# Kernel optimization log

Hardware: AMD Instinct MI355X
Metric: run time of the kernel (lower is better)

The kernel has to match this reference:

```python
import jax, jax.numpy as jnp
import numpy as np

D_CONV = 4
D_STATE = 16
DT_RANK = 64


def _silu(x):
    return x * jax.nn.sigmoid(x)


def setup_inputs() -> dict:
    key = jax.random.key(0)
    ks = jax.random.split(key, 10)
    B, L, dim = 2, 1024, 1024
    d_inner = 2 * dim
    s = lambda fan: 1.0 / np.sqrt(fan)
    inp = {
        "x": jax.random.normal(ks[0], (B, L, dim), jnp.float32),
        "ln_w": jnp.ones((dim,), jnp.float32),
        "ln_b": jnp.zeros((dim,), jnp.float32),
        "w_in": jax.random.normal(ks[1], (2 * d_inner, dim), jnp.float32) * s(dim),
        "conv_w": jax.random.normal(ks[2], (d_inner, D_CONV), jnp.float32) * s(D_CONV),
        "conv_b": jnp.zeros((d_inner,), jnp.float32),
        "w_xproj": jax.random.normal(ks[3], (DT_RANK + 2 * D_STATE, d_inner), jnp.float32) * s(d_inner),
        "w_dt": jax.random.normal(ks[4], (d_inner, DT_RANK), jnp.float32) * s(DT_RANK),
        "b_dt": jax.random.normal(ks[5], (d_inner,), jnp.float32) * 0.1,
        # S4D-real init: A = -(1..d_state) per channel
        "a_log": jnp.tile(jnp.log(jnp.arange(1, D_STATE + 1, dtype=jnp.float32)), (d_inner, 1)),
        "d_skip": jnp.ones((d_inner,), jnp.float32),
        "w_out": jax.random.normal(ks[6], (dim, d_inner), jnp.float32) * s(d_inner),
    }
    return inp


def reference(x, ln_w, ln_b, w_in, conv_w, conv_b, w_xproj, w_dt, b_dt, a_log, d_skip, w_out):
    B, L, dim = x.shape
    residual = x

    # LayerNorm
    mu = jnp.mean(x, axis=-1, keepdims=True)
    var = jnp.mean((x - mu) ** 2, axis=-1, keepdims=True)
    xn = (x - mu) * jax.lax.rsqrt(var + 1e-5) * ln_w + ln_b

    # in_proj -> (x_ssm, z) each (B, L, d_inner)
    xz = jnp.einsum("bld,ed->ble", xn, w_in)
    d_inner = xz.shape[-1] // 2
    xs, z = xz[..., :d_inner], xz[..., d_inner:]

    # depthwise causal conv1d (kernel D_CONV) + SiLU
    xp = jnp.pad(xs, ((0, 0), (D_CONV - 1, 0), (0, 0)))
    xc = conv_b
    for k in range(D_CONV):
        xc = xc + conv_w[:, k] * xp[:, k : k + L, :]
    u = _silu(xc)  # (B, L, d_inner)

    # x_proj -> dt, B, C
    x_dbl = jnp.einsum("ble,re->blr", u, w_xproj)
    dt_r = x_dbl[..., :DT_RANK]
    B_ssm = x_dbl[..., DT_RANK : DT_RANK + D_STATE]         # (B, L, n)
    C_ssm = x_dbl[..., DT_RANK + D_STATE :]                 # (B, L, n)

    dt = jax.nn.softplus(jnp.einsum("blr,er->ble", dt_r, w_dt) + b_dt)  # (B, L, d_inner)

    A = -jnp.exp(a_log)  # (d_inner, n)
    deltaA = jnp.exp(jnp.einsum("ble,en->blen", dt, A))            # (B, L, e, n)
    deltaBu = jnp.einsum("ble,bln,ble->blen", dt, B_ssm, u)        # (B, L, e, n)

    # selective scan over L
    def step(h, ins):
        dA_t, dBu_t, C_t = ins
        h = dA_t * h + dBu_t                       # (B, e, n)
        y = jnp.einsum("ben,bn->be", h, C_t)
        return h, y

    h0 = jnp.zeros((B, d_inner, D_STATE), xs.dtype)
    _, ys = jax.lax.scan(
        step,
        h0,
        (deltaA.transpose(1, 0, 2, 3), deltaBu.transpose(1, 0, 2, 3), C_ssm.transpose(1, 0, 2)),
    )
    y = ys.transpose(1, 0, 2) + u * d_skip         # (B, L, e)

    y = y * _silu(z)
    out = jnp.einsum("ble,de->bld", y, w_out)
    return residual + out
```

## Files before the change

kernel.cpp:

```cpp
#include <hip/hip_runtime.h>
#include <hip/hip_bf16.h>


#define LC 32
#define NCHUNK 32

typedef short bf16x8 __attribute__((ext_vector_type(8)));
typedef float f32x4  __attribute__((ext_vector_type(4)));

static __device__ __forceinline__ float siluf(float x) { return x / (1.f + __expf(-x)); }
static __device__ __forceinline__ unsigned short f2bf(float f) {
    unsigned int u = __float_as_uint(f);
    unsigned int r = (u + 0x7fffu + ((u >> 16) & 1u)) >> 16;
    return (unsigned short)r;
}
static __device__ __forceinline__ float bfb(unsigned short u) {
    return __uint_as_float(((unsigned int)u) << 16);
}
static __device__ __forceinline__ void gload_lds16(const void* g, void* l) {
    __builtin_amdgcn_global_load_lds(
        (const __attribute__((address_space(1))) void*)g,
        (__attribute__((address_space(3))) void*)l, 16, 0, 0);
}

__global__ __launch_bounds__(256) void f2b_all(
    const float* __restrict__ w_in,  unsigned short* __restrict__ w_in_b,
    const float* __restrict__ w_out, unsigned short* __restrict__ w_out_b,
    const float* __restrict__ w_dt,  unsigned short* __restrict__ w_dt_b)
{
    int i = blockIdx.x * 256 + threadIdx.x;
    const float* in; unsigned short* outp; int j;
    if (i < 1048576)      { in = w_in;  outp = w_in_b;  j = i; }
    else if (i < 1572864) { in = w_out; outp = w_out_b; j = i - 1048576; }
    else if (i < 1605632) { in = w_dt;  outp = w_dt_b;  j = i - 1572864; }
    else return;
    float4 v = reinterpret_cast<const float4*>(in)[j];
    ushort4 o = { f2bf(v.x), f2bf(v.y), f2bf(v.z), f2bf(v.w) };
    reinterpret_cast<ushort4*>(outp)[j] = o;
}

__global__ __launch_bounds__(256) void ln_kernel(
    const float* __restrict__ x,
    const float* __restrict__ w,
    const float* __restrict__ bias,
    unsigned short* __restrict__ xn)
{
    int m = blockIdx.x, tid = threadIdx.x;
    const float4* xr = reinterpret_cast<const float4*>(x) + (size_t)m * 256;
    float4 r = xr[tid];
    float f0 = r.x, f1 = r.y, f2 = r.z, f3 = r.w;
    float s  = f0 + f1 + f2 + f3;
    float s2 = f0*f0 + f1*f1 + f2*f2 + f3*f3;
    #pragma unroll
    for (int off = 32; off > 0; off >>= 1) {
        s  += __shfl_down(s, off);
        s2 += __shfl_down(s2, off);
    }
    __shared__ float red[8];
    if ((tid & 63) == 0) { red[tid >> 6] = s; red[4 + (tid >> 6)] = s2; }
    __syncthreads();
    float st = red[0] + red[1] + red[2] + red[3];
    float qt = red[4] + red[5] + red[6] + red[7];
    float mu   = st * (1.f / 1024.f);
    float var  = qt * (1.f / 1024.f) - mu * mu;
    float rstd = rsqrtf(var + 1e-5f);
    float4 wv = reinterpret_cast<const float4*>(w)[tid];
    float4 bv = reinterpret_cast<const float4*>(bias)[tid];
    ushort4 o = { f2bf((f0 - mu) * rstd * wv.x + bv.x),
                  f2bf((f1 - mu) * rstd * wv.y + bv.y),
                  f2bf((f2 - mu) * rstd * wv.z + bv.z),
                  f2bf((f3 - mu) * rstd * wv.w + bv.w) };
    reinterpret_cast<ushort4*>(xn + (size_t)m * 1024)[tid] = o;
}

__global__ __launch_bounds__(256) void gemm_bf16_nt(
    const unsigned short* __restrict__ A, int lda,
    const unsigned short* __restrict__ B, int ldb,
    int Kslice,
    float* __restrict__ C, unsigned short* __restrict__ Cb, int ldc,
    const float* __restrict__ bias,
    int ep, size_t Cstride)
{
    __shared__ short As[2 * 128 * 32];
    __shared__ short Bs[2 * 64 * 32];
    int tid = threadIdx.x;
    int z = blockIdx.z;
    A += (size_t)z * Kslice;
    B += (size_t)z * Kslice;
    C += (size_t)z * Cstride;
    int m0 = blockIdx.y * 128, n0 = blockIdx.x * 64;
    int lane = tid & 63, wave = tid >> 6;
    int wm = (wave >> 1) * 64, wn = (wave & 1) * 32;
    int frow = lane & 15, fq = lane >> 4;

    f32x4 acc[4][2] = {};

    int lrow = lane >> 2;
    int scol = (lane & 3) * 8;
    const unsigned short* AgL = A + (size_t)(m0 + wave * 32 + lrow) * lda + scol;
    const unsigned short* BgL = B + (size_t)(n0 + wave * 16 + lrow) * ldb + scol;
    int aoff = (wave * 32) * 32;
    int boff = (wave * 16) * 32;

    gload_lds16(AgL,                      As + aoff);
    gload_lds16(AgL + (size_t)16 * lda,   As + aoff + 16 * 32);
    gload_lds16(BgL,                      Bs + boff);

    int cur = 0;
    for (int k0 = 0; k0 < Kslice; k0 += 32) {
        __syncthreads();
        int nk = k0 + 32;
        if (nk < Kslice) {
            int nxt = cur ^ 1;
            gload_lds16(AgL + nk,                     As + nxt * 4096 + aoff);
            gload_lds16(AgL + (size_t)16 * lda + nk,  As + nxt * 4096 + aoff + 16 * 32);
            gload_lds16(BgL + nk,                     Bs + nxt * 2048 + boff);
        }
        const short* Ac = As + cur * 4096;
        const short* Bc = Bs + cur * 2048;
        bf16x8 af[4], bfr[2];
        #pragma unroll
        for (int i = 0; i < 4; ++i)
            af[i] = *reinterpret_cast<const bf16x8*>(Ac + (wm + i * 16 + frow) * 32 + fq * 8);
        #pragma unroll
        for (int j = 0; j < 2; ++j)
            bfr[j] = *reinterpret_cast<const bf16x8*>(Bc + (wn + j * 16 + frow) * 32 + fq * 8);
        #pragma unroll
        for (int i = 0; i < 4; ++i)
            #pragma unroll
            for (int j = 0; j < 2; ++j)
                acc[i][j] = __builtin_amdgcn_mfma_f32_16x16x32_bf16(af[i], bfr[j], acc[i][j], 0, 0, 0);
        cur ^= 1;
    }

    int cn = lane & 15, rq = (lane >> 4) * 4;
    #pragma unroll
    for (int i = 0; i < 4; ++i) {
        #pragma unroll
        for (int j = 0; j < 2; ++j) {
            #pragma unroll
            for (int r = 0; r < 4; ++r) {
                int row = m0 + wm + i * 16 + rq + r;
                int col = n0 + wn + j * 16 + cn;
                float v = acc[i][j][r];
                if (ep == 0) {
                    C[(size_t)row * ldc + col] = v;
                } else if (ep == 1) {
                    v += bias[col];
                    v = (v > 20.f) ? v : log1pf(__expf(v));
                    Cb[(size_t)row * ldc + col] = f2bf(v);
                } else {
                    Cb[(size_t)row * ldc + col] = f2bf(v);
                }
            }
        }
    }
}

__global__ __launch_bounds__(256) void out_reduce(
    const float* __restrict__ part, const float* __restrict__ x,
    float* __restrict__ out)
{
    int i = blockIdx.x * 256 + threadIdx.x;
    float4 s = reinterpret_cast<const float4*>(x)[i];
    #pragma unroll
    for (int z = 0; z < 4; ++z) {
        float4 p = reinterpret_cast<const float4*>(part + (size_t)z * 2097152)[i];
        s.x += p.x; s.y += p.y; s.z += p.z; s.w += p.w;
    }
    reinterpret_cast<float4*>(out)[i] = s;
}

__global__ __launch_bounds__(256) void xproj_splitk(
    const unsigned short* __restrict__ A,
    const float* __restrict__ B,
    float* __restrict__ part)
{
    __shared__ float As[16][68];
    __shared__ float Bs[16][100];
    int tid = threadIdx.x;
    int m0 = blockIdx.x * 64;
    int k0 = blockIdx.y * 128;
    int tx = tid & 15;
    int ty = tid >> 4;
    float acc[4][6] = {};
    int arow = tid >> 2, akg = (tid & 3) << 2;
    int brow1 = (256 + tid) >> 2, bkg1 = ((256 + tid) & 3) << 2;

    for (int ks = 0; ks < 128; ks += 16) {
        ushort4 au = *reinterpret_cast<const ushort4*>(A + (size_t)(m0 + arow) * 2048 + k0 + ks + akg);
        float4 av = make_float4(bfb(au.x), bfb(au.y), bfb(au.z), bfb(au.w));
        float4 bv0 = make_float4(0.f, 0.f, 0.f, 0.f), bv1 = bv0;
        if (arow < 96)  bv0 = *reinterpret_cast<const float4*>(B + (size_t)arow * 2048 + k0 + ks + akg);
        if (brow1 < 96) bv1 = *reinterpret_cast<const float4*>(B + (size_t)brow1 * 2048 + k0 + ks + bkg1);
        __syncthreads();
        As[akg + 0][arow] = av.x; As[akg + 1][arow] = av.y;
        As[akg + 2][arow] = av.z; As[akg + 3][arow] = av.w;
        if (arow < 96) {
            Bs[akg + 0][arow] = bv0.x; Bs[akg + 1][arow] = bv0.y;
            Bs[akg + 2][arow] = bv0.z; Bs[akg + 3][arow] = bv0.w;
        }
        if (brow1 < 96) {
            Bs[bkg1 + 0][brow1] = bv1.x; Bs[bkg1 + 1][brow1] = bv1.y;
            Bs[bkg1 + 2][brow1] = bv1.z; Bs[bkg1 + 3][brow1] = bv1.w;
        }
        __syncthreads();
        #pragma unroll
        for (int k = 0; k < 16; ++k) {
            float aa[4], bb[6];
            #pragma unroll
            for (int i = 0; i < 4; ++i) aa[i] = As[k][ty * 4 + i];
            #pragma unroll
            for (int j = 0; j < 6; ++j) bb[j] = Bs[k][tx * 6 + j];
            #pragma unroll
            for (int i = 0; i < 4; ++i)
                #pragma unroll
                for (int j = 0; j < 6; ++j)
                    acc[i][j] = fmaf(aa[i], bb[j], acc[i][j]);
        }
    }
    float* p = part + (size_t)blockIdx.y * 196608;
    #pragma unroll
    for (int i = 0; i < 4; ++i)
        #pragma unroll
        for (int j = 0; j < 6; ++j)
            p[(size_t)(m0 + ty * 4 + i) * 96 + tx * 6 + j] = acc[i][j];
}

__global__ __launch_bounds__(256) void xproj_reduce(
    const float* __restrict__ part, float* __restrict__ xdbl,
    unsigned short* __restrict__ dtr)
{
    int i = blockIdx.x * 256 + threadIdx.x;
    float s = 0.f;
    #pragma unroll
    for (int sd = 0; sd < 16; ++sd) s += part[(size_t)sd * 196608 + i];
    xdbl[i] = s;
    int m = i / 96, col = i - m * 96;
    if (col < 64) dtr[(size_t)m * 64 + col] = f2bf(s);
}

__global__ __launch_bounds__(256) void conv_silu_kernel(
    const unsigned short* __restrict__ xz,
    const float* __restrict__ cw,
    const float* __restrict__ cb,
    unsigned short* __restrict__ u)
{
    int idx = blockIdx.x * 256 + threadIdx.x;
    int e = idx & 2047;
    int m = idx >> 11;
    int l = m & 1023;
    float acc = cb[e];
    #pragma unroll
    for (int k = 0; k < 4; ++k) {
        int ls = l - 3 + k;
        if (ls >= 0)
            acc += cw[e * 4 + k] * bfb(xz[(size_t)(m - 3 + k) * 4096 + e]);
    }
    u[(size_t)m * 2048 + e] = f2bf(siluf(acc));
}

__global__ __launch_bounds__(256) void scan_part1(
    const unsigned short* __restrict__ dt,
    const unsigned short* __restrict__ u,
    const float* __restrict__ xdbl,
    const float* __restrict__ a_log,
    float* __restrict__ hpart,
    float* __restrict__ Aprod)
{
    int tid = threadIdx.x;
    int ch = tid >> 2, ng = tid & 3;
    int bid = blockIdx.x;
    int c = bid & 31, et = (bid >> 5) & 31, b = bid >> 10;
    int e = et * 64 + ch;
    float4 al = *reinterpret_cast<const float4*>(a_log + e * 16 + ng * 4);
    float A0 = -__expf(al.x), A1 = -__expf(al.y), A2 = -__expf(al.z), A3 = -__expf(al.w);
    size_t rbase = (size_t)b * 1024 + c * LC;
    const unsigned short* dt_p = dt + rbase * 2048 + e;
    const unsigned short* u_p  = u  + rbase * 2048 + e;
    const float* b_p  = xdbl + rbase * 96 + 64 + ng * 4;
    float h0 = 0.f, h1 = 0.f, h2 = 0.f, h3 = 0.f;
    float P0 = 1.f, P1 = 1.f, P2 = 1.f, P3 = 1.f;
    float dt_c = bfb(dt_p[0]);
    float u_c  = bfb(u_p[0]);
    float4 B_c = *reinterpret_cast<const float4*>(b_p);
    #pragma unroll 4
    for (int l = 0; l < LC; ++l) {
        float dt_n = bfb(dt_p[(size_t)(l + 1) * 2048]);
        float u_n  = bfb(u_p[(size_t)(l + 1) * 2048]);
        float4 B_n = *reinterpret_cast<const float4*>(b_p + (size_t)(l + 1) * 96);
        float du = dt_c * u_c;
        float d0 = __expf(dt_c * A0), d1 = __expf(dt_c * A1);
        float d2 = __expf(dt_c * A2), d3 = __expf(dt_c * A3);
        h0 = fmaf(d0, h0, du * B_c.x); P0 *= d0;
        h1 = fmaf(d1, h1, du * B_c.y); P1 *= d1;
        h2 = fmaf(d2, h2, du * B_c.z); P2 *= d2;
        h3 = fmaf(d3, h3, du * B_c.w); P3 *= d3;
        dt_c = dt_n; u_c = u_n; B_c = B_n;
    }
    size_t oidx = (size_t)c * 65536 + ((size_t)b * 2048 + e) * 16 + ng * 4;
    *reinterpret_cast<float4*>(hpart + oidx) = make_float4(h0, h1, h2, h3);
    *reinterpret_cast<float4*>(Aprod + oidx) = make_float4(P0, P1, P2, P3);
}

__global__ __launch_bounds__(256) void scan_combine(
    const float* __restrict__ hpart,
    const float* __restrict__ Aprod,
    float* __restrict__ hinit)
{
    int t = (blockIdx.x * 256 + threadIdx.x) * 4;
    float4 h = make_float4(0.f, 0.f, 0.f, 0.f);
    #pragma unroll
    for (int c = 0; c < NCHUNK; ++c) {
        *reinterpret_cast<float4*>(hinit + (size_t)c * 65536 + t) = h;
        float4 P = *reinterpret_cast<const float4*>(Aprod + (size_t)c * 65536 + t);
        float4 hp = *reinterpret_cast<const float4*>(hpart + (size_t)c * 65536 + t);
        h.x = fmaf(P.x, h.x, hp.x);
        h.y = fmaf(P.y, h.y, hp.y);
        h.z = fmaf(P.z, h.z, hp.z);
        h.w = fmaf(P.w, h.w, hp.w);
    }
}

__global__ __launch_bounds__(256) void scan_part2(
    const unsigned short* __restrict__ dt,
    const unsigned short* __restrict__ u,
    const float* __restrict__ xdbl,
    const unsigned short* __restrict__ xz,
    const float* __restrict__ a_log,
    const float* __restrict__ d_skip,
    const float* __restrict__ hinit,
    unsigned short* __restrict__ y)
{
    int tid = threadIdx.x;
    int ch = tid >> 2, ng = tid & 3;
    int bid = blockIdx.x;
    int c = bid & 31, et = (bid >> 5) & 31, b = bid >> 10;
    int e = et * 64 + ch;
    float4 al = *reinterpret_cast<const float4*>(a_log + e * 16 + ng * 4);
    float A0 = -__expf(al.x), A1 = -__expf(al.y), A2 = -__expf(al.z), A3 = -__expf(al.w);
    float dsk = d_skip[e];
    size_t rbase = (size_t)b * 1024 + c * LC;
    const unsigned short* dt_p = dt + rbase * 2048 + e;
    const unsigned short* u_p  = u  + rbase * 2048 + e;
    const unsigned short* z_p  = xz + rbase * 4096 + 2048 + e;
    const float* bc_p = xdbl + rbase * 96 + 64 + ng * 4;
    unsigned short* y_p = y + rbase * 2048 + e;
    size_t oidx = (size_t)c * 65536 + ((size_t)b * 2048 + e) * 16 + ng * 4;
    float4 hi = *reinterpret_cast<const float4*>(hinit + oidx);
    float h0 = hi.x, h1 = hi.y, h2 = hi.z, h3 = hi.w;
    float dt_c = bfb(dt_p[0]);
    float u_c  = bfb(u_p[0]);
    float4 B_c = *reinterpret_cast<const float4*>(bc_p);
    float4 C_c = *reinterpret_cast<const float4*>(bc_p + 16);
    #pragma unroll 4
    for (int l = 0; l < LC; ++l) {
        float dt_n = bfb(dt_p[(size_t)(l + 1) * 2048]);
        float u_n  = bfb(u_p[(size_t)(l + 1) * 2048]);
        float4 B_n = *reinterpret_cast<const float4*>(bc_p + (size_t)(l + 1) * 96);
        float4 C_n = *reinterpret_cast<const float4*>(bc_p + (size_t)(l + 1) * 96 + 16);
        float du = dt_c * u_c;
        float d0 = __expf(dt_c * A0), d1 = __expf(dt_c * A1);
        float d2 = __expf(dt_c * A2), d3 = __expf(dt_c * A3);
        h0 = fmaf(d0, h0, du * B_c.x);
        h1 = fmaf(d1, h1, du * B_c.y);
        h2 = fmaf(d2, h2, du * B_c.z);
        h3 = fmaf(d3, h3, du * B_c.w);
        float p = h0 * C_c.x + h1 * C_c.y + h2 * C_c.z + h3 * C_c.w;
        p += __shfl_xor(p, 1);
        p += __shfl_xor(p, 2);
        if (ng == 0) {
            float zv = bfb(z_p[(size_t)l * 4096]);
            y_p[(size_t)l * 2048] = f2bf((p + u_c * dsk) * siluf(zv));
        }
        dt_c = dt_n; u_c = u_n; B_c = B_n; C_c = C_n;
    }
}

extern "C" void kernel_launch(void* const* d_in, const int* in_sizes, int n_in,
                              void* d_out, int out_size, void* d_ws, size_t ws_size,
                              hipStream_t stream) {
    const float* x       = (const float*)d_in[0];
    const float* ln_w    = (const float*)d_in[1];
    const float* ln_b    = (const float*)d_in[2];
    const float* w_in    = (const float*)d_in[3];
    const float* conv_w  = (const float*)d_in[4];
    const float* conv_b  = (const float*)d_in[5];
    const float* w_xproj = (const float*)d_in[6];
    const float* w_dt    = (const float*)d_in[7];
    const float* b_dt    = (const float*)d_in[8];
    const float* a_log   = (const float*)d_in[9];
    const float* d_skip  = (const float*)d_in[10];
    const float* w_out   = (const float*)d_in[11];
    float* out = (float*)d_out;

    float* ws = (float*)d_ws;
    unsigned short* xn_b    = (unsigned short*)(ws);
    unsigned short* xz_b    = (unsigned short*)(ws + 1048576);
    unsigned short* u_b     = (unsigned short*)(ws + 5242880);
    float* xdbl  = ws + 7340032;
    unsigned short* dt_b    = (unsigned short*)(ws + 7536640);
    float* hpart = ws + 9633792;
    float* Aprod = ws + 11730944;
    float* hinit = ws + 13828096;
    unsigned short* y_b     = (unsigned short*)(ws + 15925248);
    unsigned short* w_in_b  = (unsigned short*)(ws + 18022400);
    unsigned short* w_out_b = (unsigned short*)(ws + 20119552);
    unsigned short* w_dt_b  = (unsigned short*)(ws + 21168128);
    unsigned short* dtr_b   = (unsigned short*)(ws + 21233664);
    float* xpart = ws + 9633792;
    float* opart = ws + 1048576;

    f2b_all<<<6272, 256, 0, stream>>>(w_in, w_in_b, w_out, w_out_b, w_dt, w_dt_b);
    ln_kernel<<<2048, 256, 0, stream>>>(x, ln_w, ln_b, xn_b);
    gemm_bf16_nt<<<dim3(64, 16, 1), 256, 0, stream>>>(xn_b, 1024, w_in_b, 1024, 1024,
                                                      nullptr, xz_b, 4096, nullptr, 3, 0);
    conv_silu_kernel<<<16384, 256, 0, stream>>>(xz_b, conv_w, conv_b, u_b);
    xproj_splitk<<<dim3(32, 16), 256, 0, stream>>>(u_b, w_xproj, xpart);
    xproj_reduce<<<768, 256, 0, stream>>>(xpart, xdbl, dtr_b);
    gemm_bf16_nt<<<dim3(32, 16, 1), 256, 0, stream>>>(dtr_b, 64, w_dt_b, 64, 64,
                                                      nullptr, dt_b, 2048, b_dt, 1, 0);
    scan_part1<<<2048, 256, 0, stream>>>(dt_b, u_b, xdbl, a_log, hpart, Aprod);
    scan_combine<<<64, 256, 0, stream>>>(hpart, Aprod, hinit);
    scan_part2<<<2048, 256, 0, stream>>>(dt_b, u_b, xdbl, xz_b, a_log, d_skip, hinit, y_b);
    gemm_bf16_nt<<<dim3(16, 16, 4), 256, 0, stream>>>(y_b, 2048, w_out_b, 2048, 512,
                                                      opart, nullptr, 1024, nullptr, 0, 2097152);
    out_reduce<<<2048, 256, 0, stream>>>(opart, x, out);
}
```

Baseline: 280.2 us.

## Halve scan chunk length, merge weight-cast with LayerNorm, two rows per conv thread

Scan chunk length drops from 32 to 16, so there are 64 chunks and twice as many scan blocks, which raises parallelism in the two scan passes. The cost is a longer sequential combine and larger partial buffers. The weight bf16 conversion and the LayerNorm kernels are merged into one launch to save a kernel launch. The conv+SiLU kernel now computes two consecutive rows per thread, reusing the overlapping input loads and using a vectorized load for the conv weights.

```diff
diff --git a/kernel.cpp b/kernel.cpp
--- a/kernel.cpp
+++ b/kernel.cpp
@@ -2,8 +2,8 @@
 #include <hip/hip_bf16.h>
 
 
-#define LC 32
-#define NCHUNK 32
+#define LC 16
+#define NCHUNK 64
 
 typedef short bf16x8 __attribute__((ext_vector_type(8)));
 typedef float f32x4  __attribute__((ext_vector_type(4)));
@@ -23,29 +23,29 @@
         (__attribute__((address_space(3))) void*)l, 16, 0, 0);
 }
 
-__global__ __launch_bounds__(256) void f2b_all(
+__global__ __launch_bounds__(256) void setup_kernel(
     const float* __restrict__ w_in,  unsigned short* __restrict__ w_in_b,
     const float* __restrict__ w_out, unsigned short* __restrict__ w_out_b,
-    const float* __restrict__ w_dt,  unsigned short* __restrict__ w_dt_b)
-{
-    int i = blockIdx.x * 256 + threadIdx.x;
-    const float* in; unsigned short* outp; int j;
-    if (i < 1048576)      { in = w_in;  outp = w_in_b;  j = i; }
-    else if (i < 1572864) { in = w_out; outp = w_out_b; j = i - 1048576; }
-    else if (i < 1605632) { in = w_dt;  outp = w_dt_b;  j = i - 1572864; }
-    else return;
-    float4 v = reinterpret_cast<const float4*>(in)[j];
-    ushort4 o = { f2bf(v.x), f2bf(v.y), f2bf(v.z), f2bf(v.w) };
-    reinterpret_cast<ushort4*>(outp)[j] = o;
-}
-
-__global__ __launch_bounds__(256) void ln_kernel(
+    const float* __restrict__ w_dt,  unsigned short* __restrict__ w_dt_b,
     const float* __restrict__ x,
-    const float* __restrict__ w,
-    const float* __restrict__ bias,
+    const float* __restrict__ ln_w,
+    const float* __restrict__ ln_b,
     unsigned short* __restrict__ xn)
 {
-    int m = blockIdx.x, tid = threadIdx.x;
+    int bid = blockIdx.x, tid = threadIdx.x;
+    if (bid < 6272) {
+        int i = bid * 256 + tid;
+        const float* in; unsigned short* outp; int j;
+        if (i < 1048576)      { in = w_in;  outp = w_in_b;  j = i; }
+        else if (i < 1572864) { in = w_out; outp = w_out_b; j = i - 1048576; }
+        else if (i < 1605632) { in = w_dt;  outp = w_dt_b;  j = i - 1572864; }
+        else return;
+        float4 v = reinterpret_cast<const float4*>(in)[j];
+        ushort4 o = { f2bf(v.x), f2bf(v.y), f2bf(v.z), f2bf(v.w) };
+        reinterpret_cast<ushort4*>(outp)[j] = o;
+        return;
+    }
+    int m = bid - 6272;
     const float4* xr = reinterpret_cast<const float4*>(x) + (size_t)m * 256;
     float4 r = xr[tid];
     float f0 = r.x, f1 = r.y, f2 = r.z, f3 = r.w;
@@ -64,8 +64,8 @@
     float mu   = st * (1.f / 1024.f);
     float var  = qt * (1.f / 1024.f) - mu * mu;
     float rstd = rsqrtf(var + 1e-5f);
-    float4 wv = reinterpret_cast<const float4*>(w)[tid];
-    float4 bv = reinterpret_cast<const float4*>(bias)[tid];
+    float4 wv = reinterpret_cast<const float4*>(ln_w)[tid];
+    float4 bv = reinterpret_cast<const float4*>(ln_b)[tid];
     ushort4 o = { f2bf((f0 - mu) * rstd * wv.x + bv.x),
                   f2bf((f1 - mu) * rstd * wv.y + bv.y),
                   f2bf((f2 - mu) * rstd * wv.z + bv.z),
@@ -248,16 +248,21 @@
 {
     int idx = blockIdx.x * 256 + threadIdx.x;
     int e = idx & 2047;
-    int m = idx >> 11;
-    int l = m & 1023;
-    float acc = cb[e];
-    #pragma unroll
-    for (int k = 0; k < 4; ++k) {
-        int ls = l - 3 + k;
-        if (ls >= 0)
-            acc += cw[e * 4 + k] * bfb(xz[(size_t)(m - 3 + k) * 4096 + e]);
-    }
-    u[(size_t)m * 2048 + e] = f2bf(siluf(acc));
+    int mp = idx >> 11;
+    int m0 = mp * 2;
+    int l0 = m0 & 1023;
+    float r[5];
+    #pragma unroll
+    for (int k = 0; k < 5; ++k) {
+        int lr = l0 - 3 + k;
+        r[k] = (lr >= 0) ? bfb(xz[(size_t)(m0 - 3 + k) * 4096 + e]) : 0.f;
+    }
+    float4 w = *reinterpret_cast<const float4*>(cw + e * 4);
+    float base = cb[e];
+    float a0 = base + w.x * r[0] + w.y * r[1] + w.z * r[2] + w.w * r[3];
+    float a1 = base + w.x * r[1] + w.y * r[2] + w.z * r[3] + w.w * r[4];
+    u[(size_t)m0 * 2048 + e]       = f2bf(siluf(a0));
+    u[(size_t)(m0 + 1) * 2048 + e] = f2bf(siluf(a1));
 }
 
 __global__ __launch_bounds__(256) void scan_part1(
@@ -271,7 +276,7 @@
     int tid = threadIdx.x;
     int ch = tid >> 2, ng = tid & 3;
     int bid = blockIdx.x;
-    int c = bid & 31, et = (bid >> 5) & 31, b = bid >> 10;
+    int c = bid & 63, et = (bid >> 6) & 31, b = bid >> 11;
     int e = et * 64 + ch;
     float4 al = *reinterpret_cast<const float4*>(a_log + e * 16 + ng * 4);
     float A0 = -__expf(al.x), A1 = -__expf(al.y), A2 = -__expf(al.z), A3 = -__expf(al.w);
@@ -284,7 +289,7 @@
     float dt_c = bfb(dt_p[0]);
     float u_c  = bfb(u_p[0]);
     float4 B_c = *reinterpret_cast<const float4*>(b_p);
-    #pragma unroll 4
+    #pragma unroll 8
     for (int l = 0; l < LC; ++l) {
         float dt_n = bfb(dt_p[(size_t)(l + 1) * 2048]);
         float u_n  = bfb(u_p[(size_t)(l + 1) * 2048]);
@@ -335,7 +340,7 @@
     int tid = threadIdx.x;
     int ch = tid >> 2, ng = tid & 3;
     int bid = blockIdx.x;
-    int c = bid & 31, et = (bid >> 5) & 31, b = bid >> 10;
+    int c = bid & 63, et = (bid >> 6) & 31, b = bid >> 11;
     int e = et * 64 + ch;
     float4 al = *reinterpret_cast<const float4*>(a_log + e * 16 + ng * 4);
     float A0 = -__expf(al.x), A1 = -__expf(al.y), A2 = -__expf(al.z), A3 = -__expf(al.w);
@@ -353,7 +358,7 @@
     float u_c  = bfb(u_p[0]);
     float4 B_c = *reinterpret_cast<const float4*>(bc_p);
     float4 C_c = *reinterpret_cast<const float4*>(bc_p + 16);
-    #pragma unroll 4
+    #pragma unroll 8
     for (int l = 0; l < LC; ++l) {
         float dt_n = bfb(dt_p[(size_t)(l + 1) * 2048]);
         float u_n  = bfb(u_p[(size_t)(l + 1) * 2048]);
@@ -401,28 +406,28 @@
     float* xdbl  = ws + 7340032;
     unsigned short* dt_b    = (unsigned short*)(ws + 7536640);
     float* hpart = ws + 9633792;
-    float* Aprod = ws + 11730944;
-    float* hinit = ws + 13828096;
-    unsigned short* y_b     = (unsigned short*)(ws + 15925248);
-    unsigned short* w_in_b  = (unsigned short*)(ws + 18022400);
-    unsigned short* w_out_b = (unsigned short*)(ws + 20119552);
-    unsigned short* w_dt_b  = (unsigned short*)(ws + 21168128);
-    unsigned short* dtr_b   = (unsigned short*)(ws + 21233664);
+    float* Aprod = ws + 13828096;
+    float* hinit = ws + 18022400;
+    unsigned short* y_b     = (unsigned short*)(ws + 22216704);
+    unsigned short* w_in_b  = (unsigned short*)(ws + 24313856);
+    unsigned short* w_out_b = (unsigned short*)(ws + 26411008);
+    unsigned short* w_dt_b  = (unsigned short*)(ws + 27459584);
+    unsigned short* dtr_b   = (unsigned short*)(ws + 27525120);
     float* xpart = ws + 9633792;
     float* opart = ws + 1048576;
 
-    f2b_all<<<6272, 256, 0, stream>>>(w_in, w_in_b, w_out, w_out_b, w_dt, w_dt_b);
-    ln_kernel<<<2048, 256, 0, stream>>>(x, ln_w, ln_b, xn_b);
+    setup_kernel<<<8320, 256, 0, stream>>>(w_in, w_in_b, w_out, w_out_b, w_dt, w_dt_b,
+                                           x, ln_w, ln_b, xn_b);
     gemm_bf16_nt<<<dim3(64, 16, 1), 256, 0, stream>>>(xn_b, 1024, w_in_b, 1024, 1024,
                                                       nullptr, xz_b, 4096, nullptr, 3, 0);
-    conv_silu_kernel<<<16384, 256, 0, stream>>>(xz_b, conv_w, conv_b, u_b);
+    conv_silu_kernel<<<8192, 256, 0, stream>>>(xz_b, conv_w, conv_b, u_b);
     xproj_splitk<<<dim3(32, 16), 256, 0, stream>>>(u_b, w_xproj, xpart);
     xproj_reduce<<<768, 256, 0, stream>>>(xpart, xdbl, dtr_b);
     gemm_bf16_nt<<<dim3(32, 16, 1), 256, 0, stream>>>(dtr_b, 64, w_dt_b, 64, 64,
                                                       nullptr, dt_b, 2048, b_dt, 1, 0);
-    scan_part1<<<2048, 256, 0, stream>>>(dt_b, u_b, xdbl, a_log, hpart, Aprod);
+    scan_part1<<<4096, 256, 0, stream>>>(dt_b, u_b, xdbl, a_log, hpart, Aprod);
     scan_combine<<<64, 256, 0, stream>>>(hpart, Aprod, hinit);
-    scan_part2<<<2048, 256, 0, stream>>>(dt_b, u_b, xdbl, xz_b, a_log, d_skip, hinit, y_b);
+    scan_part2<<<4096, 256, 0, stream>>>(dt_b, u_b, xdbl, xz_b, a_log, d_skip, hinit, y_b);
     gemm_bf16_nt<<<dim3(16, 16, 4), 256, 0, stream>>>(y_b, 2048, w_out_b, 2048, 512,
                                                       opart, nullptr, 1024, nullptr, 0, 2097152);
     out_reduce<<<2048, 256, 0, stream>>>(opart, x, out);
```

Measured after the change: 275.9 us. Within noise of the previous version (-1.5%).
